# Performance work log

Measured on AMD Instinct MI355X. Metric: run time of the kernel, lower is better.

The kernel has to match this reference:

```python
import jax, jax.numpy as jnp
import numpy as np
import math

D_MODEL = 1024
NUM_HEADS = 16
D_HEAD = D_MODEL // NUM_HEADS          # 64
N_FREQ = D_HEAD // 2 + 1               # 33 rfft bins
COMPRESSION_RATIO = 0.5


def setup_inputs() -> dict:
    key = jax.random.key(0)
    k_x, k_qkv, k_out, k_b, k_m = jax.random.split(key, 5)
    B, S = 2, 2048
    x = jax.random.normal(k_x, (B, S, D_MODEL), dtype=jnp.float32)
    # Linear weights stored as [in, out] (torch Linear uses [out, in]; math identical).
    w_qkv = jax.random.normal(k_qkv, (D_MODEL, 3 * D_MODEL), dtype=jnp.float32) / math.sqrt(D_MODEL)
    w_out = jax.random.normal(k_out, (D_MODEL, D_MODEL), dtype=jnp.float32) / math.sqrt(D_MODEL)
    b_out = jax.random.normal(k_b, (D_MODEL,), dtype=jnp.float32) * 0.01
    # Learned per-frequency-bin mask logits of AdaptiveFrequencyMask(d_state=d_head).
    # Initialized around logit(compression_ratio) with small noise.
    init_logit = math.log(COMPRESSION_RATIO / (1.0 - COMPRESSION_RATIO))
    mask_logits = init_logit + 0.1 * jax.random.normal(k_m, (N_FREQ,), dtype=jnp.float32)
    return {"x": x, "w_qkv": w_qkv, "w_out": w_out, "b_out": b_out, "mask_logits": mask_logits}


def _spectral_filter(t, mask):
    # rfft over d_head dim, apply learned soft mask, inverse rfft.  t: [B,H,S,dh]
    tf = jnp.fft.rfft(t, axis=-1)          # [B,H,S,N_FREQ] complex
    tf = tf * mask                          # broadcast real mask over bins
    return jnp.fft.irfft(tf, n=t.shape[-1], axis=-1).astype(t.dtype)


def reference(x, w_qkv, w_out, b_out, mask_logits):
    B, S, D = x.shape
    H, dh = NUM_HEADS, D_HEAD
    qkv = x @ w_qkv                                         # [B,S,3D]
    q, k, v = jnp.split(qkv, 3, axis=-1)
    # [B,S,D] -> [B,H,S,dh]
    to_heads = lambda t: t.reshape(B, S, H, dh).transpose(0, 2, 1, 3)
    q, k, v = to_heads(q), to_heads(k), to_heads(v)
    mask = jax.nn.sigmoid(mask_logits)                      # [N_FREQ]
    q = _spectral_filter(q, mask)
    k = _spectral_filter(k, mask)
    scores = jnp.einsum('bhqd,bhkd->bhqk', q, k) / math.sqrt(dh)
    attn = jax.nn.softmax(scores, axis=-1)                  # dropout p=0 (eval)
    out = jnp.einsum('bhqk,bhkd->bhqd', attn, v)
    out = out.transpose(0, 2, 1, 3).reshape(B, S, D)
    return out @ w_out + b_out
```

## Files before the change

kernel.cpp:

```cpp
#include <hip/hip_runtime.h>

#define S_LEN 2048
#define NH    16
#define DH    64
#define DM    1024
#define NQKV  3072

typedef __attribute__((ext_vector_type(8))) __bf16 bf16x8;
typedef __attribute__((ext_vector_type(4))) float  f32x4;
typedef unsigned short ushort_t;

static __device__ __forceinline__ unsigned short bf16b(float f) {
  return __builtin_bit_cast(unsigned short, (__bf16)f);
}

static __device__ __forceinline__ float exp2v(float x) {
  return __builtin_amdgcn_exp2f(x);
}

static __device__ __forceinline__ bf16x8 pack8(float4 f0, float4 f1) {
  uint4 v;
  v.x = ((unsigned)bf16b(f0.y) << 16) | bf16b(f0.x);
  v.y = ((unsigned)bf16b(f0.w) << 16) | bf16b(f0.z);
  v.z = ((unsigned)bf16b(f1.y) << 16) | bf16b(f1.x);
  v.w = ((unsigned)bf16b(f1.w) << 16) | bf16b(f1.z);
  return __builtin_bit_cast(bf16x8, v);
}

static __device__ __forceinline__ void glds16(const void* g, void* l) {
  __builtin_amdgcn_global_load_lds((const __attribute__((address_space(1))) unsigned int*)g,
                                   (__attribute__((address_space(3))) unsigned int*)l, 16, 0, 0);
}

#define OFF_WT  65536ull
#define OFF_WOT 6356992ull
#define OFF_Q   8454144ull
#define OFF_K   16842752ull
#define OFF_V   25231360ull
#define OFF_AO  33619968ull

__global__ __launch_bounds__(256) void k_prep(const float* __restrict__ wqkv,
                                              const float* __restrict__ wout,
                                              const float* __restrict__ x,
                                              const float* __restrict__ logits,
                                              unsigned short* __restrict__ Wt,
                                              unsigned short* __restrict__ Wot,
                                              unsigned short* __restrict__ xb) {
  __shared__ __align__(16) char sbuf[16640];
  int bid = blockIdx.x;
  int t = threadIdx.x;

  if (bid < 256) {
    float* msk = (float*)sbuf;
    float* Kd  = (float*)(sbuf + 144);
    ushort_t (*Fb)[72] = (ushort_t(*)[72])(sbuf + 416);
    if (t < 33) msk[t] = 1.0f / (1.0f + __expf(-logits[t]));
    __syncthreads();
    if (t < 64) {
      float acc = msk[0];
      #pragma unroll
      for (int f = 1; f < 32; ++f) {
        int r = (f * t) & 63;
        acc += 2.0f * msk[f] * __cosf((float)r * (6.28318530717958647692f / 64.0f));
      }
      acc += msk[32] * ((t & 1) ? -1.0f : 1.0f);
      Kd[t] = acc * (1.0f / 64.0f);
    }
    __syncthreads();
    for (int idx = t; idx < 4096; idx += 256) {
      int j = idx >> 6, i = idx & 63;
      Fb[j][i] = bf16b(Kd[(j - i) & 63]);
    }
    __syncthreads();

    int lane = t & 63, w = t >> 6;
    int m16 = lane & 15, quad = lane >> 4;
    int kx = bid >> 5, yy = bid & 31;
    int which = yy >> 4, h = yy & 15;
    int base = which * 1024 + h * 64;

    bf16x8 af0 = *(const bf16x8*)(&Fb[w * 16 + m16][quad * 8]);
    bf16x8 af1 = *(const bf16x8*)(&Fb[w * 16 + m16][32 + quad * 8]);

    f32x4 acc[8] = {};
    #pragma unroll 2
    for (int n = 0; n < 8; ++n) {
      const float* Wg = wqkv + (size_t)(kx * 128 + n * 16 + m16) * NQKV + base + quad * 8;
      float4 a0 = *(const float4*)(Wg);
      float4 a1 = *(const float4*)(Wg + 4);
      float4 b0 = *(const float4*)(Wg + 32);
      float4 b1 = *(const float4*)(Wg + 36);
      acc[n] = __builtin_amdgcn_mfma_f32_16x16x32_bf16(af0, pack8(a0, a1), acc[n], 0, 0, 0);
      acc[n] = __builtin_amdgcn_mfma_f32_16x16x32_bf16(af1, pack8(b0, b1), acc[n], 0, 0, 0);
    }
    float sc = (which == 0) ? 0.18033688011112042f : 1.0f;
    #pragma unroll
    for (int n = 0; n < 8; ++n) {
      #pragma unroll
      for (int r = 0; r < 4; ++r) {
        int j = w * 16 + quad * 4 + r;
        Wt[(size_t)(base + j) * DM + kx * 128 + n * 16 + m16] = bf16b(acc[n][r] * sc);
      }
    }
  } else if (bid < 768) {
    float (*Ts)[65] = (float(*)[65])sbuf;
    int b1 = bid - 256;
    if (b1 < 256) {
      int kt = b1 & 15, nt = b1 >> 4;
      int cb = 2048 + nt * 64, kbase = kt * 64;
      #pragma unroll
      for (int p = 0; p < 16; ++p) {
        int kk = p * 4 + (t >> 6);
        Ts[kk][t & 63] = wqkv[(size_t)(kbase + kk) * NQKV + cb + (t & 63)];
      }
      __syncthreads();
      #pragma unroll
      for (int p = 0; p < 16; ++p) {
        int nn = p * 4 + (t >> 6);
        Wt[(size_t)(cb + nn) * DM + kbase + (t & 63)] = bf16b(Ts[t & 63][nn]);
      }
    } else {
      int b2 = b1 - 256;
      int kt = b2 & 15, nt = b2 >> 4;
      int cb = nt * 64, kbase = kt * 64;
      #pragma unroll
      for (int p = 0; p < 16; ++p) {
        int kk = p * 4 + (t >> 6);
        Ts[kk][t & 63] = wout[(size_t)(kbase + kk) * DM + cb + (t & 63)];
      }
      __syncthreads();
      #pragma unroll
      for (int p = 0; p < 16; ++p) {
        int nn = p * 4 + (t >> 6);
        Wot[(size_t)(cb + nn) * DM + kbase + (t & 63)] = bf16b(Ts[t & 63][nn]);
      }
    }
  } else {
    size_t i = ((size_t)(bid - 768) * 256 + t) * 8;
    const float4* xp = (const float4*)(x + i);
    float4 a = xp[0], b = xp[1];
    uint4 v;
    v.x = ((unsigned)bf16b(a.y) << 16) | bf16b(a.x);
    v.y = ((unsigned)bf16b(a.w) << 16) | bf16b(a.z);
    v.z = ((unsigned)bf16b(b.y) << 16) | bf16b(b.x);
    v.w = ((unsigned)bf16b(b.w) << 16) | bf16b(b.z);
    *(uint4*)(xb + i) = v;
  }
}

__device__ __forceinline__ void gemm_core_async(const unsigned short* __restrict__ A,
                                                const unsigned short* __restrict__ Bw,
                                                int bm, int bn, unsigned short* smem,
                                                f32x4 (&acc)[4][4]) {
  unsigned short* As = smem;
  unsigned short* Bs = smem + 8192;
  int t = threadIdx.x, lane = t & 63, w = t >> 6;
  int m16 = lane & 15, quad = lane >> 4;
  int wr = (w >> 1) * 64, wc = (w & 1) * 64;
  int lr = lane >> 3, lc = lane & 7;
  int gc = lc ^ lr;
  int xr = m16 & 7;
  const unsigned short* Agb = A  + (size_t)(bm * 128) * DM + gc * 8;
  const unsigned short* Bgb = Bw + (size_t)(bn * 128) * DM + gc * 8;

  for (int k0 = 0; k0 < DM; k0 += 64) {
    #pragma unroll
    for (int p = 0; p < 4; ++p) {
      int row = p * 32 + w * 8 + lr;
      glds16(Agb + (size_t)row * DM + k0, As + row * 64 + lc * 8);
      glds16(Bgb + (size_t)row * DM + k0, Bs + row * 64 + lc * 8);
    }
    __syncthreads();
    #pragma unroll
    for (int kk = 0; kk < 2; ++kk) {
      bf16x8 af[4], bfr[4];
      #pragma unroll
      for (int i = 0; i < 4; ++i)
        af[i] = *(const bf16x8*)(As + (wr + i * 16 + m16) * 64 + ((kk * 4 + quad) ^ xr) * 8);
      #pragma unroll
      for (int j = 0; j < 4; ++j)
        bfr[j] = *(const bf16x8*)(Bs + (wc + j * 16 + m16) * 64 + ((kk * 4 + quad) ^ xr) * 8);
      #pragma unroll
      for (int i = 0; i < 4; ++i)
        #pragma unroll
        for (int j = 0; j < 4; ++j)
          acc[i][j] = __builtin_amdgcn_mfma_f32_16x16x32_bf16(af[i], bfr[j], acc[i][j], 0, 0, 0);
    }
    __syncthreads();
  }
}

__global__ __launch_bounds__(256) void k_gemm_qkv(const unsigned short* __restrict__ xb,
                                                  const unsigned short* __restrict__ Bw,
                                                  unsigned short* __restrict__ Qb,
                                                  unsigned short* __restrict__ Kb,
                                                  unsigned short* __restrict__ Vt) {
  __shared__ __align__(16) unsigned short smem[18432];
  f32x4 acc[4][4] = {};
  int bn = blockIdx.x, bm = blockIdx.y;
  gemm_core_async(xb, Bw, bm, bn, smem, acc);

  int t = threadIdx.x, lane = t & 63, w = t >> 6;
  int m16 = lane & 15, quad = lane >> 4;
  int wr = (w >> 1) * 64, wc = (w & 1) * 64;
  int b = bm >> 4, srow = (bm & 15) * 128;
  int which = bn >> 3;
  ushort_t (*Tr)[130] = (ushort_t(*)[130])smem;
  if (which < 2) {
    #pragma unroll
    for (int i = 0; i < 4; ++i)
      #pragma unroll
      for (int j = 0; j < 4; ++j)
        #pragma unroll
        for (int r = 0; r < 4; ++r)
          Tr[wr + i * 16 + quad * 4 + r][wc + j * 16 + m16] = bf16b(acc[i][j][r]);
    __syncthreads();
    int row = t >> 1, half = t & 1;
    int cloc = bn * 128 + half * 64 - which * 1024;
    int h = cloc >> 6;
    unsigned short* dst = (which ? Kb : Qb) +
        ((size_t)(b * 16 + h) * 2048 + srow + row) * 64;
    #pragma unroll
    for (int p = 0; p < 8; ++p)
      *(uint4*)(dst + p * 8) = *(const uint4*)(&Tr[row][half * 64 + p * 8]);
  } else {
    #pragma unroll
    for (int i = 0; i < 4; ++i)
      #pragma unroll
      for (int j = 0; j < 4; ++j)
        #pragma unroll
        for (int r = 0; r < 4; ++r)
          Tr[wc + j * 16 + m16][wr + i * 16 + quad * 4 + r] = bf16b(acc[i][j][r]);
    __syncthreads();
    int dl = t >> 1, half = t & 1;
    int cloc = (bn - 16) * 128 + dl;
    int h = cloc >> 6, d = cloc & 63;
    unsigned short* dst = Vt + ((size_t)(b * 16 + h) * 64 + d) * 2048 + srow + half * 64;
    #pragma unroll
    for (int p = 0; p < 8; ++p)
      *(uint4*)(dst + p * 8) = *(const uint4*)(&Tr[dl][half * 64 + p * 8]);
  }
}

__global__ __launch_bounds__(512, 2) void k_attn(const unsigned short* __restrict__ Qb,
                                                 const unsigned short* __restrict__ Kb,
                                                 const unsigned short* __restrict__ Vt,
                                                 unsigned short* __restrict__ AO) {
  __shared__ __align__(16) unsigned short smem[65536];
  int t = threadIdx.x;
  int w = t >> 6, lane = t & 63;
  int m16 = lane & 15, quad = lane >> 4;
  int bid = blockIdx.x;
  int jj = bid >> 3;
  int bh = ((jj & 3) << 3) + (bid & 7);
  int qbase = (jj >> 2) * 256 + w * 32;

  const unsigned short* QpA = Qb + ((size_t)bh * S_LEN + qbase + m16) * DH + quad * 8;
  const unsigned short* QpB = QpA + 16 * DH;
  bf16x8 aq0A = *(const bf16x8*)(QpA);
  bf16x8 aq1A = *(const bf16x8*)(QpA + 32);
  bf16x8 aq0B = *(const bf16x8*)(QpB);
  bf16x8 aq1B = *(const bf16x8*)(QpB + 32);
  const unsigned short* Kbase = Kb + (size_t)bh * S_LEN * DH;
  const unsigned short* Vbase = Vt + (size_t)bh * DH * S_LEN;

  int xr = m16 & 7;
  unsigned short* Pw = smem + 32768 + w * 4096;

  int trow = t >> 3;
  int tcol = t & 7;
  int gswz = tcol ^ (trow & 7);
  const unsigned short* Kg = Kbase + (size_t)trow * 64 + gswz * 8;
  const unsigned short* Vg = Vbase + (size_t)trow * S_LEN + gswz * 8;
  unsigned short* Kl = smem + trow * 64 + tcol * 8;
  unsigned short* Vl = smem + 16384 + trow * 64 + tcol * 8;

  f32x4 oA[4] = {}, oB[4] = {};
  float lA = 0.f, lB = 0.f;
  f32x4 zero = {0.f, 0.f, 0.f, 0.f};

  #pragma unroll
  for (int tt = 0; tt < 4; ++tt) {
    glds16(Kg + (size_t)tt * 4096, Kl + tt * 4096);
    glds16(Vg + tt * 64,           Vl + tt * 4096);
  }

  #pragma unroll 1
  for (int wnd = 0; wnd < 16; ++wnd) {
    if (wnd < 15) asm volatile("s_waitcnt vmcnt(4)" ::: "memory");
    else          asm volatile("s_waitcnt vmcnt(0)" ::: "memory");
    __builtin_amdgcn_s_barrier();
    __builtin_amdgcn_sched_barrier(0);
    int sb = (wnd & 1) << 1;
    const unsigned short* Ka  = smem + sb * 4096;
    const unsigned short* Kbs = smem + (sb + 1) * 4096;
    const unsigned short* Va  = smem + 16384 + sb * 4096;
    const unsigned short* Vbs = smem + 16384 + (sb + 1) * 4096;
    unsigned short* Pa = Pw;
    unsigned short* Pb = Pw + 2048;

    f32x4 saA[4], saB[4];
    #pragma unroll
    for (int g = 0; g < 4; ++g) {
      int rk = g * 16 + m16;
      bf16x8 kf0 = *(const bf16x8*)(Ka + rk * 64 + ((quad ^ xr) * 8));
      bf16x8 kf1 = *(const bf16x8*)(Ka + rk * 64 + (((4 + quad) ^ xr) * 8));
      saA[g] = __builtin_amdgcn_mfma_f32_16x16x32_bf16(kf0, aq0A, zero, 0, 0, 0);
      saA[g] = __builtin_amdgcn_mfma_f32_16x16x32_bf16(kf1, aq1A, saA[g], 0, 0, 0);
      saB[g] = __builtin_amdgcn_mfma_f32_16x16x32_bf16(kf0, aq0B, zero, 0, 0, 0);
      saB[g] = __builtin_amdgcn_mfma_f32_16x16x32_bf16(kf1, aq1B, saB[g], 0, 0, 0);
    }
    #pragma unroll
    for (int g = 0; g < 4; ++g) {
      int chw = (((2 * g + (quad >> 1)) ^ xr) << 3) + ((quad & 1) << 2);
      float a0 = exp2v(saA[g][0]), a1 = exp2v(saA[g][1]);
      float a2 = exp2v(saA[g][2]), a3 = exp2v(saA[g][3]);
      lA += (a0 + a1) + (a2 + a3);
      uint2 pka;
      pka.x = ((unsigned)bf16b(a1) << 16) | bf16b(a0);
      pka.y = ((unsigned)bf16b(a3) << 16) | bf16b(a2);
      *(uint2*)(Pa + m16 * 64 + chw) = pka;
      float b0 = exp2v(saB[g][0]), b1 = exp2v(saB[g][1]);
      float b2 = exp2v(saB[g][2]), b3 = exp2v(saB[g][3]);
      lB += (b0 + b1) + (b2 + b3);
      uint2 pkb;
      pkb.x = ((unsigned)bf16b(b1) << 16) | bf16b(b0);
      pkb.y = ((unsigned)bf16b(b3) << 16) | bf16b(b2);
      *(uint2*)(Pa + (16 + m16) * 64 + chw) = pkb;
    }
    f32x4 sbA[4], sbB[4];
    #pragma unroll
    for (int g = 0; g < 4; ++g) {
      int rk = g * 16 + m16;
      bf16x8 kf0 = *(const bf16x8*)(Kbs + rk * 64 + ((quad ^ xr) * 8));
      bf16x8 kf1 = *(const bf16x8*)(Kbs + rk * 64 + (((4 + quad) ^ xr) * 8));
      sbA[g] = __builtin_amdgcn_mfma_f32_16x16x32_bf16(kf0, aq0A, zero, 0, 0, 0);
      sbA[g] = __builtin_amdgcn_mfma_f32_16x16x32_bf16(kf1, aq1A, sbA[g], 0, 0, 0);
      sbB[g] = __builtin_amdgcn_mfma_f32_16x16x32_bf16(kf0, aq0B, zero, 0, 0, 0);
      sbB[g] = __builtin_amdgcn_mfma_f32_16x16x32_bf16(kf1, aq1B, sbB[g], 0, 0, 0);
    }
    #pragma unroll
    for (int c = 0; c < 2; ++c) {
      bf16x8 apA = *(const bf16x8*)(Pa + m16 * 64 + (((4 * c + quad) ^ xr) << 3));
      bf16x8 apB = *(const bf16x8*)(Pa + (16 + m16) * 64 + (((4 * c + quad) ^ xr) << 3));
      #pragma unroll
      for (int j = 0; j < 4; ++j) {
        int dv = j * 16 + m16;
        bf16x8 bv = *(const bf16x8*)(Va + dv * 64 + (((c * 4 + quad) ^ xr) * 8));
        oA[j] = __builtin_amdgcn_mfma_f32_16x16x32_bf16(apA, bv, oA[j], 0, 0, 0);
        oB[j] = __builtin_amdgcn_mfma_f32_16x16x32_bf16(apB, bv, oB[j], 0, 0, 0);
      }
    }
    #pragma unroll
    for (int g = 0; g < 4; ++g) {
      int chw = (((2 * g + (quad >> 1)) ^ xr) << 3) + ((quad & 1) << 2);
      float a0 = exp2v(sbA[g][0]), a1 = exp2v(sbA[g][1]);
      float a2 = exp2v(sbA[g][2]), a3 = exp2v(sbA[g][3]);
      lA += (a0 + a1) + (a2 + a3);
      uint2 pka;
      pka.x = ((unsigned)bf16b(a1) << 16) | bf16b(a0);
      pka.y = ((unsigned)bf16b(a3) << 16) | bf16b(a2);
      *(uint2*)(Pb + m16 * 64 + chw) = pka;
      float b0 = exp2v(sbB[g][0]), b1 = exp2v(sbB[g][1]);
      float b2 = exp2v(sbB[g][2]), b3 = exp2v(sbB[g][3]);
      lB += (b0 + b1) + (b2 + b3);
      uint2 pkb;
      pkb.x = ((unsigned)bf16b(b1) << 16) | bf16b(b0);
      pkb.y = ((unsigned)bf16b(b3) << 16) | bf16b(b2);
      *(uint2*)(Pb + (16 + m16) * 64 + chw) = pkb;
    }
    #pragma unroll
    for (int c = 0; c < 2; ++c) {
      bf16x8 apA = *(const bf16x8*)(Pb + m16 * 64 + (((4 * c + quad) ^ xr) << 3));
      bf16x8 apB = *(const bf16x8*)(Pb + (16 + m16) * 64 + (((4 * c + quad) ^ xr) << 3));
      #pragma unroll
      for (int j = 0; j < 4; ++j) {
        int dv = j * 16 + m16;
        bf16x8 bv = *(const bf16x8*)(Vbs + dv * 64 + (((c * 4 + quad) ^ xr) * 8));
        oA[j] = __builtin_amdgcn_mfma_f32_16x16x32_bf16(apA, bv, oA[j], 0, 0, 0);
        oB[j] = __builtin_amdgcn_mfma_f32_16x16x32_bf16(apB, bv, oB[j], 0, 0, 0);
      }
    }
    if (wnd < 14) {
      __builtin_amdgcn_s_barrier();
      int ta = 2 * wnd + 4;
      glds16(Kg + (size_t)ta * 4096,       Kl + sb * 4096);
      glds16(Vg + ta * 64,                 Vl + sb * 4096);
      glds16(Kg + (size_t)(ta + 1) * 4096, Kl + (sb + 1) * 4096);
      glds16(Vg + (ta + 1) * 64,           Vl + (sb + 1) * 4096);
    }
  }

  lA += __shfl_xor(lA, 16); lA += __shfl_xor(lA, 32);
  lB += __shfl_xor(lB, 16); lB += __shfl_xor(lB, 32);
  float ivA = 1.0f / lA;
  float ivB = 1.0f / lB;
  int b = bh >> 4, h = bh & 15;
  #pragma unroll
  for (int r = 0; r < 4; ++r) {
    float vA = __shfl(ivA, quad * 4 + r);
    float vB = __shfl(ivB, quad * 4 + r);
    size_t row0 = (size_t)b * S_LEN + qbase + quad * 4 + r;
    unsigned short* d0 = AO + row0 * DM + h * DH + m16;
    unsigned short* d1 = AO + (row0 + 16) * DM + h * DH + m16;
    #pragma unroll
    for (int j = 0; j < 4; ++j) {
      d0[j * 16] = bf16b(oA[j][r] * vA);
      d1[j * 16] = bf16b(oB[j][r] * vB);
    }
  }
}

__global__ __launch_bounds__(256) void k_gemm_out(const unsigned short* __restrict__ A,
                                                  const unsigned short* __restrict__ Bw,
                                                  const float* __restrict__ bias,
                                                  float* __restrict__ out) {
  __shared__ __align__(16) unsigned short smem[18432];
  f32x4 acc[4][4] = {};
  int bn = blockIdx.x, bm = blockIdx.y;
  gemm_core_async(A, Bw, bm, bn, smem, acc);

  int t = threadIdx.x, lane = t & 63, w = t >> 6;
  int m16 = lane & 15, quad = lane >> 4;
  int wr = (w >> 1) * 64, wc = (w & 1) * 64;
  #pragma unroll
  for (int i = 0; i < 4; ++i) {
    int grow = bm * 128 + wr + i * 16 + quad * 4;
    #pragma unroll
    for (int j = 0; j < 4; ++j) {
      int gc = bn * 128 + wc + j * 16 + m16;
      float bb = bias[gc];
      #pragma unroll
      for (int r = 0; r < 4; ++r)
        out[(size_t)(grow + r) * DM + gc] = acc[i][j][r] + bb;
    }
  }
}

extern "C" void kernel_launch(void* const* d_in, const int* in_sizes, int n_in,
                              void* d_out, int out_size, void* d_ws, size_t ws_size,
                              hipStream_t stream) {
  const float* x    = (const float*)d_in[0];
  const float* wqkv = (const float*)d_in[1];
  const float* wout = (const float*)d_in[2];
  const float* bout = (const float*)d_in[3];
  const float* mlog = (const float*)d_in[4];
  char* ws = (char*)d_ws;
  unsigned short* Wt  = (unsigned short*)(ws + OFF_WT);
  unsigned short* Wot = (unsigned short*)(ws + OFF_WOT);
  unsigned short* Qb  = (unsigned short*)(ws + OFF_Q);
  unsigned short* Kb  = (unsigned short*)(ws + OFF_K);
  unsigned short* Vt  = (unsigned short*)(ws + OFF_V);
  unsigned short* xb  = (unsigned short*)(ws + OFF_AO);
  unsigned short* AO  = (unsigned short*)(ws + OFF_AO);
  float* out = (float*)d_out;

  k_prep<<<dim3(2816), dim3(256), 0, stream>>>(wqkv, wout, x, mlog, Wt, Wot, xb);
  k_gemm_qkv<<<dim3(24, 32), dim3(256), 0, stream>>>(xb, Wt, Qb, Kb, Vt);
  k_attn<<<dim3(256), dim3(512), 0, stream>>>(Qb, Kb, Vt, AO);
  k_gemm_out<<<dim3(8, 32), dim3(256), 0, stream>>>(AO, Wot, bout, out);
}
```

Before: 196.7 us.

## Multi-stage prefetch pipeline for async-LDS GEMM core

Replaces the load-sync-compute-sync loop in the shared GEMM core with a 4-stage LDS ring. Two 64-wide K slices are consumed per window while the next two are issued as direct global-to-LDS loads, with vmcnt waits and raw barriers controlling overlap. The aim is to hide global load latency behind MFMA work in both the QKV and output projections. In exchange LDS per block grows to 128KB, which limits occupancy to one block per CU, and the hand-written waitcnt/barrier logic is fragile.

```diff
diff --git a/kernel.cpp b/kernel.cpp
--- a/kernel.cpp
+++ b/kernel.cpp
@@ -152,8 +152,6 @@
                                                 const unsigned short* __restrict__ Bw,
                                                 int bm, int bn, unsigned short* smem,
                                                 f32x4 (&acc)[4][4]) {
-  unsigned short* As = smem;
-  unsigned short* Bs = smem + 8192;
   int t = threadIdx.x, lane = t & 63, w = t >> 6;
   int m16 = lane & 15, quad = lane >> 4;
   int wr = (w >> 1) * 64, wc = (w & 1) * 64;
@@ -162,32 +160,62 @@
   int xr = m16 & 7;
   const unsigned short* Agb = A  + (size_t)(bm * 128) * DM + gc * 8;
   const unsigned short* Bgb = Bw + (size_t)(bn * 128) * DM + gc * 8;
-
-  for (int k0 = 0; k0 < DM; k0 += 64) {
+  int srow = w * 8 + lr;
+  unsigned short* Al = smem + srow * 64 + lc * 8;
+  unsigned short* Bl = smem + 8192 + srow * 64 + lc * 8;
+
+  #pragma unroll
+  for (int s = 0; s < 4; ++s) {
     #pragma unroll
     for (int p = 0; p < 4; ++p) {
-      int row = p * 32 + w * 8 + lr;
-      glds16(Agb + (size_t)row * DM + k0, As + row * 64 + lc * 8);
-      glds16(Bgb + (size_t)row * DM + k0, Bs + row * 64 + lc * 8);
-    }
-    __syncthreads();
-    #pragma unroll
-    for (int kk = 0; kk < 2; ++kk) {
-      bf16x8 af[4], bfr[4];
-      #pragma unroll
-      for (int i = 0; i < 4; ++i)
-        af[i] = *(const bf16x8*)(As + (wr + i * 16 + m16) * 64 + ((kk * 4 + quad) ^ xr) * 8);
-      #pragma unroll
-      for (int j = 0; j < 4; ++j)
-        bfr[j] = *(const bf16x8*)(Bs + (wc + j * 16 + m16) * 64 + ((kk * 4 + quad) ^ xr) * 8);
-      #pragma unroll
-      for (int i = 0; i < 4; ++i)
+      int row = p * 32 + srow;
+      glds16(Agb + (size_t)row * DM + s * 64, Al + s * 16384 + p * 2048);
+      glds16(Bgb + (size_t)row * DM + s * 64, Bl + s * 16384 + p * 2048);
+    }
+  }
+
+  #pragma unroll 1
+  for (int wnd = 0; wnd < 8; ++wnd) {
+    if (wnd < 7) asm volatile("s_waitcnt vmcnt(16)" ::: "memory");
+    else         asm volatile("s_waitcnt vmcnt(0)" ::: "memory");
+    __builtin_amdgcn_s_barrier();
+    __builtin_amdgcn_sched_barrier(0);
+    int sb = (wnd & 1) << 1;
+    #pragma unroll
+    for (int half = 0; half < 2; ++half) {
+      const unsigned short* As = smem + (sb + half) * 16384;
+      const unsigned short* Bs = As + 8192;
+      #pragma unroll
+      for (int kk = 0; kk < 2; ++kk) {
+        bf16x8 af[4], bfr[4];
+        #pragma unroll
+        for (int i = 0; i < 4; ++i)
+          af[i] = *(const bf16x8*)(As + (wr + i * 16 + m16) * 64 + ((kk * 4 + quad) ^ xr) * 8);
         #pragma unroll
         for (int j = 0; j < 4; ++j)
-          acc[i][j] = __builtin_amdgcn_mfma_f32_16x16x32_bf16(af[i], bfr[j], acc[i][j], 0, 0, 0);
-    }
-    __syncthreads();
-  }
+          bfr[j] = *(const bf16x8*)(Bs + (wc + j * 16 + m16) * 64 + ((kk * 4 + quad) ^ xr) * 8);
+        #pragma unroll
+        for (int i = 0; i < 4; ++i)
+          #pragma unroll
+          for (int j = 0; j < 4; ++j)
+            acc[i][j] = __builtin_amdgcn_mfma_f32_16x16x32_bf16(af[i], bfr[j], acc[i][j], 0, 0, 0);
+      }
+    }
+    if (wnd < 6) {
+      __builtin_amdgcn_s_barrier();
+      int ka = 2 * wnd + 4;
+      #pragma unroll
+      for (int half = 0; half < 2; ++half) {
+        #pragma unroll
+        for (int p = 0; p < 4; ++p) {
+          int row = p * 32 + srow;
+          glds16(Agb + (size_t)row * DM + (ka + half) * 64, Al + (sb + half) * 16384 + p * 2048);
+          glds16(Bgb + (size_t)row * DM + (ka + half) * 64, Bl + (sb + half) * 16384 + p * 2048);
+        }
+      }
+    }
+  }
+  __syncthreads();
 }
 
 __global__ __launch_bounds__(256) void k_gemm_qkv(const unsigned short* __restrict__ xb,
@@ -195,7 +223,7 @@
                                                   unsigned short* __restrict__ Qb,
                                                   unsigned short* __restrict__ Kb,
                                                   unsigned short* __restrict__ Vt) {
-  __shared__ __align__(16) unsigned short smem[18432];
+  __shared__ __align__(16) unsigned short smem[65536];
   f32x4 acc[4][4] = {};
   int bn = blockIdx.x, bm = blockIdx.y;
   gemm_core_async(xb, Bw, bm, bn, smem, acc);
@@ -415,7 +443,7 @@
                                                   const unsigned short* __restrict__ Bw,
                                                   const float* __restrict__ bias,
                                                   float* __restrict__ out) {
-  __shared__ __align__(16) unsigned short smem[18432];
+  __shared__ __align__(16) unsigned short smem[65536];
   f32x4 acc[4][4] = {};
   int bn = blockIdx.x, bm = blockIdx.y;
   gemm_core_async(A, Bw, bm, bn, smem, acc);
```

Result: faster. 187.0 us (-5.0%).
